# Kernel optimization log

Hardware: AMD Instinct MI355X
Metric: run time of the kernel (lower is better)

## Reference

```python
import jax, jax.numpy as jnp
import numpy as np

S, E, K, D = 50000, 20000, 128, 64
NUM_LAYER = 3
E1, E0 = 1000000, 1000000  # nnz of pos / neg adjacency
B = 4096


def _edges(key, n_rows, n_cols, n_edges):
    k1, k2, k3 = jax.random.split(key, 3)
    rows = jax.random.randint(k1, (n_edges,), 0, n_rows)
    cols = jax.random.randint(k2, (n_edges,), 0, n_cols)
    vals = jax.random.uniform(k3, (n_edges,), jnp.float32, 0.0, 0.1)
    return rows, cols, vals


def setup_inputs() -> dict:
    key = jax.random.key(0)
    ks = jax.random.split(key, 32)
    inp = {}
    inp['stu_id'] = jax.random.randint(ks[0], (B,), 0, S)
    inp['exer_id'] = jax.random.randint(ks[1], (B,), 0, E)
    inp['kn_emb'] = (jax.random.uniform(ks[2], (B, K)) < 0.1).astype(jnp.float32)
    # embeddings
    inp['stu_emb'] = jax.random.normal(ks[3], (S, D), jnp.float32) * 0.1
    inp['exer_emb'] = jax.random.normal(ks[4], (E, D), jnp.float32) * 0.1
    inp['kn_base'] = jax.random.normal(ks[5], (K, D), jnp.float32) * 0.1
    inp['stu_bias'] = jax.random.normal(ks[6], (S, 1), jnp.float32) * 0.1
    inp['e_disc'] = jax.random.normal(ks[7], (E, 1), jnp.float32) * 0.1
    # GCN linear layers
    inp['W1_w'] = jax.random.normal(ks[8], (K, K), jnp.float32) * (1.0 / np.sqrt(K))
    inp['W1_b'] = jnp.zeros((K,), jnp.float32)
    inp['W0_w'] = jax.random.normal(ks[9], (K, K), jnp.float32) * (1.0 / np.sqrt(K))
    inp['W0_b'] = jnp.zeros((K,), jnp.float32)
    # PosLinear prednet
    inp['pn1_w'] = jax.random.normal(ks[10], (256, K), jnp.float32) * 0.05
    inp['pn1_b'] = jnp.zeros((256,), jnp.float32)
    inp['pn2_w'] = jax.random.normal(ks[11], (128, 256), jnp.float32) * 0.05
    inp['pn2_b'] = jnp.zeros((128,), jnp.float32)
    inp['pn3_w'] = jax.random.normal(ks[12], (1, 128), jnp.float32) * 0.05
    inp['pn3_b'] = jnp.zeros((1,), jnp.float32)
    # sparse adjacencies (COO) pos(1) / neg(0), user->item and item->user
    r, c, v = _edges(ks[13], S, E, E1)
    inp['ui1_r'], inp['ui1_c'], inp['ui1_v'] = r, c, v
    r, c, v = _edges(ks[14], E, S, E1)
    inp['iu1_r'], inp['iu1_c'], inp['iu1_v'] = r, c, v
    r, c, v = _edges(ks[15], S, E, E0)
    inp['ui0_r'], inp['ui0_c'], inp['ui0_v'] = r, c, v
    r, c, v = _edges(ks[16], E, S, E0)
    inp['iu0_r'], inp['iu0_c'], inp['iu0_v'] = r, c, v
    # self-loop degree normalizers (1/(deg+1)-style positive scalars)
    inp['d_i_1'] = jax.random.uniform(ks[17], (S,), jnp.float32, 0.01, 1.0)
    inp['d_j_1'] = jax.random.uniform(ks[18], (E,), jnp.float32, 0.01, 1.0)
    inp['d_i_0'] = jax.random.uniform(ks[19], (S,), jnp.float32, 0.01, 1.0)
    inp['d_j_0'] = jax.random.uniform(ks[20], (E,), jnp.float32, 0.01, 1.0)
    return inp


def _spmm(rows, cols, vals, x, n_rows):
    # sparse [n_rows, n_cols] @ dense [n_cols, K]
    return jax.ops.segment_sum(vals[:, None] * x[cols], rows, num_segments=n_rows)


def _poslinear(x, w, b):
    wp = 2.0 * jax.nn.relu(-w) + w  # == |w|, as in PosLinear
    return x @ wp.T + b


def reference(stu_id, exer_id, kn_emb, stu_emb, exer_emb, kn_base, stu_bias, e_disc,
              W1_w, W1_b, W0_w, W0_b, pn1_w, pn1_b, pn2_w, pn2_b, pn3_w, pn3_b,
              ui1_r, ui1_c, ui1_v, iu1_r, iu1_c, iu1_v,
              ui0_r, ui0_c, ui0_v, iu0_r, iu0_c, iu0_v,
              d_i_1, d_j_1, d_i_0, d_j_0):
    # project embeddings onto knowledge space: [S,K], [E,K]
    stat = stu_emb @ kn_base.T
    kdiff = exer_emb @ kn_base.T
    for _ in range(NUM_LAYER):
        u1 = _spmm(ui1_r, ui1_c, ui1_v, kdiff, S) + stat * d_i_1[:, None]
        u1 = u1 @ W1_w.T + W1_b
        i1 = _spmm(iu1_r, iu1_c, iu1_v, stat, E) + kdiff * d_j_1[:, None]
        i1 = i1 @ W1_w.T + W1_b
        u0 = _spmm(ui0_r, ui0_c, ui0_v, kdiff, S) + stat * d_i_0[:, None]
        u0 = u0 @ W0_w.T + W0_b
        i0 = _spmm(iu0_r, iu0_c, iu0_v, stat, E) + kdiff * d_j_0[:, None]
        i0 = i0 @ W0_w.T + W0_b
        stat = u1 + u0
        kdiff = i1 + i0
    # diagnosis head (NCD-style), dropout in eval mode -> identity
    stat_b = jax.nn.sigmoid(stat[stu_id] + stu_bias[stu_id])      # [B,K]
    k_d = jax.nn.sigmoid(kdiff[exer_id])                           # [B,K]
    disc = jax.nn.sigmoid(e_disc[exer_id])                         # [B,1]
    x = disc * (stat_b - k_d) * kn_emb
    x = jax.nn.sigmoid(_poslinear(x, pn1_w, pn1_b))
    x = jax.nn.sigmoid(_poslinear(x, pn2_w, pn2_b))
    out = jax.nn.sigmoid(_poslinear(x, pn3_w, pn3_b)).reshape(-1)
    return out
```

## Files before the change

### kernel.cpp

```cpp
#include <hip/hip_runtime.h>
#include <hip/hip_bf16.h>

#define SN 50000
#define EN 20000
#define KN 128
#define DN 64
#define BN 4096
#define NE 1000000
#define NLAYER 3

#define CH_SHIFT 12
#define NCH0 5
#define NCH1 13
#define SIDE1_BASE2 (2 * SN * NCH0)
#define NTOT2 (2 * (SN * NCH0 + EN * NCH1))

#define BIN_SHIFT 11
#define NBIN2 ((NTOT2 + 2047) >> 11)
#define T1 4096
#define PG1 ((NE + T1 - 1) / T1)
#define HB 256

typedef float f32x4 __attribute__((ext_vector_type(4)));
typedef float f32x2 __attribute__((ext_vector_type(2)));
typedef short bf16x8 __attribute__((ext_vector_type(8)));

__device__ __forceinline__ float sigmoidf_(float v) { return 1.f / (1.f + __expf(-v)); }
__device__ __forceinline__ float bf_lo(unsigned u) { return __uint_as_float(u << 16); }
__device__ __forceinline__ float bf_hi(unsigned u) { return __uint_as_float(u & 0xffff0000u); }
__device__ __forceinline__ float bf_one(unsigned short s) { return __uint_as_float((unsigned)s << 16); }
__device__ __forceinline__ unsigned packbf2(float a, float b) {
    __hip_bfloat16 ha = __float2bfloat16(a), hb = __float2bfloat16(b);
    unsigned short ua = *(unsigned short*)&ha, ub = *(unsigned short*)&hb;
    return (unsigned)ua | ((unsigned)ub << 16);
}
__device__ __forceinline__ unsigned short packbf1(float a) {
    __hip_bfloat16 ha = __float2bfloat16(a);
    return *(unsigned short*)&ha;
}

struct CsrB {
    const int* rows[4]; const int* cols[4]; const float* vals[4];
};

__device__ __forceinline__ int bucket_idx(int a, int r, int cc) {
    int side = a >> 1;
    int nch = side ? NCH1 : NCH0;
    int base = side ? SIDE1_BASE2 : 0;
    int tb = a & 1;
    return base + (2 * r + tb) * nch + (cc >> CH_SHIFT);
}

__global__ __launch_bounds__(256) void hist_coarse(CsrB c, int* __restrict__ cnt) {
    __shared__ int h[512];
    const int t = threadIdx.x;
    h[t] = 0; h[t + 256] = 0;
    __syncthreads();
    const int a = blockIdx.x >> 8;
    const int tile = blockIdx.x & 255;
    const int per = (NE + HB - 1) / HB;
    const int beg = tile * per, end = min(beg + per, NE);
    for (int i = beg + t; i < end; i += 256)
        atomicAdd(&h[bucket_idx(a, c.rows[a][i], c.cols[a][i]) >> BIN_SHIFT], 1);
    __syncthreads();
    if (h[t]) atomicAdd(&cnt[t], h[t]);
    if (h[t + 256]) atomicAdd(&cnt[t + 256], h[t + 256]);
}

__global__ __launch_bounds__(512) void scan_coarse(const int* __restrict__ cnt,
                                                   int* __restrict__ base,
                                                   int* __restrict__ tails) {
    __shared__ int sh[512];
    const int t = threadIdx.x;
    const int v = (t < NBIN2) ? cnt[t] : 0;
    sh[t] = v;
    __syncthreads();
    for (int o = 1; o < 512; o <<= 1) {
        int x = sh[t]; int u = (t >= o) ? sh[t - o] : 0;
        __syncthreads(); sh[t] = x + u; __syncthreads();
    }
    if (t < NBIN2) {
        const int ex = sh[t] - v;
        base[t] = ex;
        tails[t] = ex;
    }
    if (t == 511) base[NBIN2] = sh[511];
}

__global__ __launch_bounds__(512) void part1(CsrB c, int* __restrict__ tails,
                                             int2* __restrict__ stg) {
    __shared__ int2 srec[T1];
    __shared__ unsigned short sbin[T1];
    __shared__ int h[512], offs[512], gbase[512], sc[512];
    const int t = threadIdx.x;
    const int a = blockIdx.x / PG1;
    const int tile = blockIdx.x - a * PG1;
    const int beg = tile * T1;
    const int cnt = min(T1, NE - beg);
    h[t] = 0;
    __syncthreads();

    int2 rec[8]; int rbin[8]; int rrank[8];
#pragma unroll
    for (int k = 0; k < 8; ++k) {
        int o = t + k * 512;
        if (o < cnt) {
            int i = beg + o;
            int cc = c.cols[a][i];
            int B = bucket_idx(a, c.rows[a][i], cc);
            int bin = B >> BIN_SHIFT;
            rec[k] = make_int2(cc | ((B & 2047) << 17), __float_as_int(c.vals[a][i]));
            rbin[k] = bin;
            rrank[k] = atomicAdd(&h[bin], 1);
        } else {
            rbin[k] = -1;
        }
    }
    __syncthreads();
    sc[t] = h[t];
    __syncthreads();
    for (int o = 1; o < 512; o <<= 1) {
        int x = sc[t]; int u = (t >= o) ? sc[t - o] : 0;
        __syncthreads(); sc[t] = x + u; __syncthreads();
    }
    offs[t] = sc[t] - h[t];
    if (h[t] > 0) gbase[t] = atomicAdd(&tails[t], h[t]);
    __syncthreads();
#pragma unroll
    for (int k = 0; k < 8; ++k) {
        if (rbin[k] >= 0) {
            int pos = offs[rbin[k]] + rrank[k];
            srec[pos] = rec[k];
            sbin[pos] = (unsigned short)rbin[k];
        }
    }
    __syncthreads();
    for (int idx = t; idx < cnt; idx += 512) {
        int b = sbin[idx];
        stg[gbase[b] + (idx - offs[b])] = srec[idx];
    }
}

__global__ __launch_bounds__(512) void part2(const int* __restrict__ coarseBase,
                                             const int2* __restrict__ stg,
                                             int* __restrict__ rp,
                                             int2* __restrict__ cv) {
    __shared__ int cnt2[2048];
    __shared__ int tsum[512];
    const int b = blockIdx.x;
    const int t = threadIdx.x;
    const int fineBase = b << BIN_SHIFT;
    const int nf = min(2048, NTOT2 - fineBase);
    const int segBeg = coarseBase[b];
    const int segEnd = coarseBase[b + 1];
    for (int i = t; i < 2048; i += 512) cnt2[i] = 0;
    __syncthreads();
    for (int e = segBeg + t; e < segEnd; e += 512)
        atomicAdd(&cnt2[((unsigned)stg[e].x) >> 17], 1);
    __syncthreads();
    const int i4 = t * 4;
    int v0 = cnt2[i4], v1 = cnt2[i4 + 1], v2 = cnt2[i4 + 2], v3 = cnt2[i4 + 3];
    tsum[t] = v0 + v1 + v2 + v3;
    __syncthreads();
    for (int o = 1; o < 512; o <<= 1) {
        int x = tsum[t]; int u = (t >= o) ? tsum[t - o] : 0;
        __syncthreads(); tsum[t] = x + u; __syncthreads();
    }
    const int pre = (t == 0) ? 0 : tsum[t - 1];
    const int p0 = pre, p1 = pre + v0, p2 = p1 + v1, p3 = p2 + v2;
    cnt2[i4] = p0; cnt2[i4 + 1] = p1; cnt2[i4 + 2] = p2; cnt2[i4 + 3] = p3;
    if (i4 + 0 < nf) rp[fineBase + i4 + 0] = segBeg + p0;
    if (i4 + 1 < nf) rp[fineBase + i4 + 1] = segBeg + p1;
    if (i4 + 2 < nf) rp[fineBase + i4 + 2] = segBeg + p2;
    if (i4 + 3 < nf) rp[fineBase + i4 + 3] = segBeg + p3;
    if (b == NBIN2 - 1 && t == 511) rp[NTOT2] = segEnd;
    __syncthreads();
    for (int e = segBeg + t; e < segEnd; e += 512) {
        int2 r = stg[e];
        int pos = segBeg + atomicAdd(&cnt2[((unsigned)r.x) >> 17], 1);
        cv[pos] = make_int2(r.x & 0xFFFF, r.y);
    }
}

__global__ __launch_bounds__(256) void f2bf(const float* __restrict__ src,
                                            unsigned short* __restrict__ dst, int n2) {
    int i = blockIdx.x * 256 + threadIdx.x;
    if (i < n2) {
        float2 f = ((const float2*)src)[i];
        ((unsigned*)dst)[i] = packbf2(f.x, f.y);
    }
}

__global__ __launch_bounds__(256) void bf2fp8(const unsigned* __restrict__ src,
                                              unsigned* __restrict__ dst, int n4) {
    int i = blockIdx.x * 256 + threadIdx.x;
    if (i < n4) {
        unsigned a = src[2 * i], b = src[2 * i + 1];
        float f0 = bf_lo(a), f1 = bf_hi(a), f2 = bf_lo(b), f3 = bf_hi(b);
        int pk = __builtin_amdgcn_cvt_pk_fp8_f32(f0, f1, 0, false);
        pk = __builtin_amdgcn_cvt_pk_fp8_f32(f2, f3, pk, true);
        dst[i] = (unsigned)pk;
    }
}

template <int KK>
__global__ __launch_bounds__(256) void gemm_proj(const float* __restrict__ X,
                                                 const unsigned short* __restrict__ W,
                                                 unsigned short* __restrict__ out, int M) {
    constexpr int PITCH = KK + 8;
    __shared__ unsigned short Wl[128 * PITCH];
    const int t = threadIdx.x;
    for (int idx = t * 8; idx < 128 * KK; idx += 2048) {
        int r = idx / KK, k = idx - r * KK;
        *(uint4*)(&Wl[r * PITCH + k]) = *(const uint4*)(&W[idx]);
    }
    __syncthreads();
    const int lane = t & 63;
    const int nm = lane & 15;
    const int quad = lane >> 4;
    const int row0 = blockIdx.x * 64 + (t >> 6) * 16;
    if (row0 >= M) return;

    f32x4 acc[8];
#pragma unroll
    for (int nt = 0; nt < 8; ++nt) acc[nt] = (f32x4){0.f, 0.f, 0.f, 0.f};

    const float* xrow = X + (size_t)(row0 + nm) * KK + quad * 8;
#pragma unroll
    for (int ks = 0; ks < KK / 32; ++ks) {
        float4 f0 = *(const float4*)(xrow + ks * 32);
        float4 f1 = *(const float4*)(xrow + ks * 32 + 4);
        unsigned q[4] = {packbf2(f0.x, f0.y), packbf2(f0.z, f0.w),
                         packbf2(f1.x, f1.y), packbf2(f1.z, f1.w)};
        bf16x8 a = *(bf16x8*)q;
#pragma unroll
        for (int nt = 0; nt < 8; ++nt) {
            bf16x8 b = *(const bf16x8*)(&Wl[(nt * 16 + nm) * PITCH + ks * 32 + quad * 8]);
            acc[nt] = __builtin_amdgcn_mfma_f32_16x16x32_bf16(a, b, acc[nt], 0, 0, 0);
        }
    }
    unsigned short* orow = out + (size_t)(row0 + quad * 4) * 128 + nm;
#pragma unroll
    for (int r = 0; r < 4; ++r)
#pragma unroll
        for (int nt = 0; nt < 8; ++nt)
            orow[(size_t)r * 128 + nt * 16] = packbf1(acc[nt][r]);
}

template <bool LIST>
__global__ __launch_bounds__(256) void gemm2_mfma(
    const unsigned short* __restrict__ agg1S, const unsigned short* __restrict__ agg0S,
    const unsigned short* __restrict__ yS,
    const float* __restrict__ d1S, const float* __restrict__ d0S,
    unsigned short* __restrict__ outS,
    const unsigned short* __restrict__ agg1E, const unsigned short* __restrict__ agg0E,
    const unsigned short* __restrict__ yE,
    const float* __restrict__ d1E, const float* __restrict__ d0E,
    unsigned short* __restrict__ outE,
    const unsigned short* __restrict__ W1, const unsigned short* __restrict__ W0,
    const float* __restrict__ b1, const float* __restrict__ b0,
    const int* __restrict__ idsS, const int* __restrict__ idsE, int nblkS) {
    constexpr int PITCH = 136;
    __shared__ unsigned short Wl[2 * 128 * PITCH];
    const int t = threadIdx.x;
    for (int idx = t * 8; idx < 128 * 128; idx += 2048) {
        int r = idx >> 7, k = idx & 127;
        *(uint4*)(&Wl[r * PITCH + k]) = *(const uint4*)(&W1[idx]);
        *(uint4*)(&Wl[128 * PITCH + r * PITCH + k]) = *(const uint4*)(&W0[idx]);
    }
    __syncthreads();
    const bool sideE = (int)blockIdx.x >= nblkS;
    const unsigned short* agg1 = sideE ? agg1E : agg1S;
    const unsigned short* agg0 = sideE ? agg0E : agg0S;
    const unsigned short* y    = sideE ? yE : yS;
    const float* d1 = sideE ? d1E : d1S;
    const float* d0 = sideE ? d0E : d0S;
    unsigned short* out = sideE ? outE : outS;
    const int M = LIST ? BN : (sideE ? EN : SN);
    const int lane = t & 63;
    const int nm = lane & 15;
    const int quad = lane >> 4;
    const int row0 = ((int)blockIdx.x - (sideE ? nblkS : 0)) * 64 + (t >> 6) * 16;
    if (row0 >= M) return;

    const int lrow = row0 + nm;
    int grow = lrow;
    if (LIST) grow = (sideE ? idsE : idsS)[lrow];

    const float d1v = d1[grow];
    const float d0v = d0[grow];

    f32x4 acc[8];
#pragma unroll
    for (int nt = 0; nt < 8; ++nt) acc[nt] = (f32x4){0.f, 0.f, 0.f, 0.f};

    const size_t rbA = (size_t)lrow * 128 + quad * 8;
    const size_t rbY = (size_t)grow * 128 + quad * 8;
#pragma unroll
    for (int ks = 0; ks < 4; ++ks) {
        uint4 ua1 = *(const uint4*)(agg1 + rbA + ks * 32);
        uint4 ua0 = *(const uint4*)(agg0 + rbA + ks * 32);
        uint4 uy  = *(const uint4*)(y    + rbY + ks * 32);
        uint4 p1, p0;
        {
            unsigned* a1 = (unsigned*)&ua1; unsigned* a0 = (unsigned*)&ua0;
            unsigned* yy = (unsigned*)&uy;
            unsigned* q1 = (unsigned*)&p1; unsigned* q0 = (unsigned*)&p0;
#pragma unroll
            for (int w = 0; w < 4; ++w) {
                float ylo = bf_lo(yy[w]), yhi = bf_hi(yy[w]);
                q1[w] = packbf2(bf_lo(a1[w]) + d1v * ylo, bf_hi(a1[w]) + d1v * yhi);
                q0[w] = packbf2(bf_lo(a0[w]) + d0v * ylo, bf_hi(a0[w]) + d0v * yhi);
            }
        }
        bf16x8 af1 = *(bf16x8*)&p1;
        bf16x8 af0 = *(bf16x8*)&p0;
#pragma unroll
        for (int nt = 0; nt < 8; ++nt) {
            bf16x8 bw1 = *(const bf16x8*)(&Wl[(nt * 16 + nm) * PITCH + ks * 32 + quad * 8]);
            acc[nt] = __builtin_amdgcn_mfma_f32_16x16x32_bf16(af1, bw1, acc[nt], 0, 0, 0);
            bf16x8 bw0 = *(const bf16x8*)(&Wl[128 * PITCH + (nt * 16 + nm) * PITCH + ks * 32 + quad * 8]);
            acc[nt] = __builtin_amdgcn_mfma_f32_16x16x32_bf16(af0, bw0, acc[nt], 0, 0, 0);
        }
    }
    unsigned short* orow = out + (size_t)(row0 + quad * 4) * 128 + nm;
#pragma unroll
    for (int nt = 0; nt < 8; ++nt) {
        float bb = b1[nt * 16 + nm] + b0[nt * 16 + nm];
#pragma unroll
        for (int r = 0; r < 4; ++r)
            orow[(size_t)r * 128 + nt * 16] = packbf1(acc[nt][r] + bb);
    }
}

template <bool LIST>
__global__ __launch_bounds__(256) void spmm_all(
    const int* __restrict__ rp, const long long* __restrict__ cv,
    const unsigned char* __restrict__ kd8, const unsigned char* __restrict__ st8,
    unsigned short* __restrict__ as1, unsigned short* __restrict__ as0,
    unsigned short* __restrict__ ae1, unsigned short* __restrict__ ae0,
    const int* __restrict__ idsS, const int* __restrict__ idsE) {
    const int wave = (blockIdx.x * 256 + threadIdx.x) >> 6;
    const int lane = threadIdx.x & 63;
    const int NW = LIST ? 2 * BN : SN + EN;
    if (wave >= NW) return;
    const bool sideE = LIST ? (wave >= BN) : (wave >= SN);
    const int li = sideE ? (wave - (LIST ? BN : SN)) : wave;
    const int r = LIST ? (sideE ? idsE[li] : idsS[li]) : li;
    const int nch = sideE ? NCH1 : NCH0;
    const int* rpb = rp + (sideE ? SIDE1_BASE2 : 0);
    const int q = lane >> 4;
    const int c = lane & 15;
    const unsigned char* g8 = (sideE ? st8 : kd8) + c * 8;

    const int rbase = 2 * r * nch;
    const int e0 = rpb[rbase];
    const int em = rpb[rbase + nch];
    const int ee = rpb[rbase + 2 * nch];

    f32x2 accP[4], accN[4];
#pragma unroll
    for (int j = 0; j < 4; ++j) { accP[j] = (f32x2){0.f, 0.f}; accN[j] = (f32x2){0.f, 0.f}; }

#define QUAD(E, ACC)                                                        \
    {                                                                       \
        int col = (int)((E) & 0xFFFF);                                      \
        float v = __int_as_float((int)((E) >> 32));                         \
        f32x2 vv = {v, v};                                                  \
        uint2 u = *(const uint2*)(g8 + (col << 7));                         \
        ACC[0] += vv * __builtin_amdgcn_cvt_pk_f32_fp8((int)u.x, false);    \
        ACC[1] += vv * __builtin_amdgcn_cvt_pk_f32_fp8((int)u.x, true);     \
        ACC[2] += vv * __builtin_amdgcn_cvt_pk_f32_fp8((int)u.y, false);    \
        ACC[3] += vv * __builtin_amdgcn_cvt_pk_f32_fp8((int)u.y, true);     \
    }

    {
        int e = e0;
        for (; e + 16 <= em; e += 16) {
            long long E0 = cv[e + q];
            long long E1 = cv[e + 4 + q];
            long long E2 = cv[e + 8 + q];
            long long E3 = cv[e + 12 + q];
            QUAD(E0, accP) QUAD(E1, accP) QUAD(E2, accP) QUAD(E3, accP)
        }
        for (; e + 4 <= em; e += 4) {
            long long E0 = cv[e + q];
            QUAD(E0, accP)
        }
        if (e < em) {
            int idx = min(e + q, em - 1);
            long long E0 = cv[idx];
            if (e + q >= em) E0 &= 0xFFFFLL;
            QUAD(E0, accP)
        }
    }
    {
        int e = em;
        for (; e + 16 <= ee; e += 16) {
            long long E0 = cv[e + q];
            long long E1 = cv[e + 4 + q];
            long long E2 = cv[e + 8 + q];
            long long E3 = cv[e + 12 + q];
            QUAD(E0, accN) QUAD(E1, accN) QUAD(E2, accN) QUAD(E3, accN)
        }
        for (; e + 4 <= ee; e += 4) {
            long long E0 = cv[e + q];
            QUAD(E0, accN)
        }
        if (e < ee) {
            int idx = min(e + q, ee - 1);
            long long E0 = cv[idx];
            if (e + q >= ee) E0 &= 0xFFFFLL;
            QUAD(E0, accN)
        }
    }
#undef QUAD

#pragma unroll
    for (int j = 0; j < 4; ++j) {
        accP[j].x += __shfl_xor(accP[j].x, 16);
        accP[j].y += __shfl_xor(accP[j].y, 16);
        accN[j].x += __shfl_xor(accN[j].x, 16);
        accN[j].y += __shfl_xor(accN[j].y, 16);
        accP[j].x += __shfl_xor(accP[j].x, 32);
        accP[j].y += __shfl_xor(accP[j].y, 32);
        accN[j].x += __shfl_xor(accN[j].x, 32);
        accN[j].y += __shfl_xor(accN[j].y, 32);
    }
    unsigned short* o1 = sideE ? ae1 : as1;
    unsigned short* o0 = sideE ? ae0 : as0;
    const int oi = LIST ? li : r;
    const int base = (oi << 7) + c * 8;
    if (q == 0) {
        uint4 w;
        w.x = packbf2(accP[0].x, accP[0].y);
        w.y = packbf2(accP[1].x, accP[1].y);
        w.z = packbf2(accP[2].x, accP[2].y);
        w.w = packbf2(accP[3].x, accP[3].y);
        *(uint4*)&o1[base] = w;
    } else if (q == 1) {
        uint4 w;
        w.x = packbf2(accN[0].x, accN[0].y);
        w.y = packbf2(accN[1].x, accN[1].y);
        w.z = packbf2(accN[2].x, accN[2].y);
        w.w = packbf2(accN[3].x, accN[3].y);
        *(uint4*)&o0[base] = w;
    }
}

template <int KK, int NCOLS, int ROWS, bool ABSW, bool SIG>
__global__ __launch_bounds__(256) void gemm_xwT(const float* __restrict__ X,
                                                const float* __restrict__ W,
                                                const float* __restrict__ bias,
                                                float* __restrict__ out, int M) {
    constexpr int KP = 32;
    constexpr int NG = 256 / NCOLS;
    constexpr int RT = ROWS / NG;
    __shared__ float BT[KP * (NCOLS + 1)];
    __shared__ float Xl[ROWS * (KK + 1)];
    const int t = threadIdx.x;
    const int j = t % NCOLS;
    const int rg = t / NCOLS;
    const int row0 = blockIdx.x * ROWS;

    for (int idx = t; idx < ROWS * KK; idx += 256) {
        int r = idx / KK, k = idx % KK;
        int gr = row0 + r;
        Xl[r * (KK + 1) + k] = (gr < M) ? X[gr * KK + k] : 0.f;
    }
    float acc[RT];
#pragma unroll
    for (int i = 0; i < RT; ++i) acc[i] = 0.f;

    for (int k0 = 0; k0 < KK; k0 += KP) {
        __syncthreads();
        for (int idx = t; idx < NCOLS * KP; idx += 256) {
            int jj = idx / KP, kp = idx % KP;
            float w = W[jj * KK + k0 + kp];
            BT[kp * (NCOLS + 1) + jj] = ABSW ? fabsf(w) : w;
        }
        __syncthreads();
#pragma unroll
        for (int kp = 0; kp < KP; ++kp) {
            float b = BT[kp * (NCOLS + 1) + j];
#pragma unroll
            for (int rr = 0; rr < RT; ++rr)
                acc[rr] += Xl[(rg * RT + rr) * (KK + 1) + k0 + kp] * b;
        }
    }
    float bj = bias ? bias[j] : 0.f;
#pragma unroll
    for (int rr = 0; rr < RT; ++rr) {
        int gr = row0 + rg * RT + rr;
        if (gr < M) {
            float v = acc[rr] + bj;
            out[gr * NCOLS + j] = SIG ? sigmoidf_(v) : v;
        }
    }
}

__global__ __launch_bounds__(128) void head1_kernel(
    const int* __restrict__ stu_id, const int* __restrict__ exer_id,
    const float* __restrict__ kn_emb, const unsigned short* __restrict__ statB,
    const unsigned short* __restrict__ kdB, const float* __restrict__ stu_bias,
    const float* __restrict__ e_disc, float* __restrict__ x) {
    const int b = blockIdx.x;
    const int k = threadIdx.x;
    const int sid = stu_id[b], eid = exer_id[b];
    float disc = sigmoidf_(e_disc[eid]);
    float sb = sigmoidf_(bf_one(statB[(b << 7) + k]) + stu_bias[sid]);
    float kd = sigmoidf_(bf_one(kdB[(b << 7) + k]));
    x[(b << 7) + k] = disc * (sb - kd) * kn_emb[(b << 7) + k];
}

__global__ __launch_bounds__(256) void pn3_kernel(const float* __restrict__ h2,
                                                  const float* __restrict__ w3,
                                                  const float* __restrict__ b3,
                                                  float* __restrict__ out) {
    __shared__ float wl[128];
    const int t = threadIdx.x;
    if (t < 128) wl[t] = fabsf(w3[t]);
    __syncthreads();
    const int b = blockIdx.x * 256 + t;
    float acc = 0.f;
#pragma unroll 4
    for (int k = 0; k < 128; ++k) acc += h2[(b << 7) + k] * wl[k];
    out[b] = sigmoidf_(acc + b3[0]);
}

static inline size_t align256(size_t x) { return (x + 255) & ~size_t(255); }

extern "C" void kernel_launch(void* const* d_in, const int* in_sizes, int n_in,
                              void* d_out, int out_size, void* d_ws, size_t ws_size,
                              hipStream_t stream) {
    const int*   stu_id   = (const int*)d_in[0];
    const int*   exer_id  = (const int*)d_in[1];
    const float* kn_emb   = (const float*)d_in[2];
    const float* stu_emb  = (const float*)d_in[3];
    const float* exer_emb = (const float*)d_in[4];
    const float* kn_base  = (const float*)d_in[5];
    const float* stu_bias = (const float*)d_in[6];
    const float* e_disc   = (const float*)d_in[7];
    const float* W1_w     = (const float*)d_in[8];
    const float* W1_b     = (const float*)d_in[9];
    const float* W0_w     = (const float*)d_in[10];
    const float* W0_b     = (const float*)d_in[11];
    const float* pn1_w    = (const float*)d_in[12];
    const float* pn1_b    = (const float*)d_in[13];
    const float* pn2_w    = (const float*)d_in[14];
    const float* pn2_b    = (const float*)d_in[15];
    const float* pn3_w    = (const float*)d_in[16];
    const float* pn3_b    = (const float*)d_in[17];
    const int*   ui1_r = (const int*)d_in[18]; const int* ui1_c = (const int*)d_in[19];
    const float* ui1_v = (const float*)d_in[20];
    const int*   iu1_r = (const int*)d_in[21]; const int* iu1_c = (const int*)d_in[22];
    const float* iu1_v = (const float*)d_in[23];
    const int*   ui0_r = (const int*)d_in[24]; const int* ui0_c = (const int*)d_in[25];
    const float* ui0_v = (const float*)d_in[26];
    const int*   iu0_r = (const int*)d_in[27]; const int* iu0_c = (const int*)d_in[28];
    const float* iu0_v = (const float*)d_in[29];
    const float* d_i_1 = (const float*)d_in[30];
    const float* d_j_1 = (const float*)d_in[31];
    const float* d_i_0 = (const float*)d_in[32];
    const float* d_j_0 = (const float*)d_in[33];
    float* out = (float*)d_out;

    typedef unsigned short u16;
    typedef unsigned char u8;
    char* p = (char*)d_ws;
    size_t off = 0;
    auto alloc = [&](size_t bytes) { char* q = p + off; off += align256(bytes); return q; };
    u16* stat  = (u16*)alloc(size_t(SN) * KN * 2);
    u16* kdiff = (u16*)alloc(size_t(EN) * KN * 2);
    u8* st8 = (u8*)alloc(size_t(SN) * KN);
    u8* kd8 = (u8*)alloc(size_t(EN) * KN);
    u16* as1 = (u16*)alloc(size_t(SN) * KN * 2);
    u16* as0 = (u16*)alloc(size_t(SN) * KN * 2);
    u16* ae1 = (u16*)alloc(size_t(EN) * KN * 2);
    u16* ae0 = (u16*)alloc(size_t(EN) * KN * 2);
    u16* statB = (u16*)alloc(size_t(BN) * KN * 2);
    u16* kdB   = (u16*)alloc(size_t(BN) * KN * 2);
    u16* Kb  = (u16*)alloc(size_t(KN) * DN * 2);
    u16* Wb1 = (u16*)alloc(size_t(KN) * KN * 2);
    u16* Wb0 = (u16*)alloc(size_t(KN) * KN * 2);
    int*  coarseCnt  = (int*)alloc(512 * 4);
    int*  coarseBase = (int*)alloc((NBIN2 + 1) * 4);
    int*  tails      = (int*)alloc(512 * 4);
    int*  rp_all     = (int*)alloc(size_t(NTOT2 + 1) * 4);
    int2* stg        = (int2*)alloc(size_t(4) * NE * 8);
    int2* cv_all     = (int2*)alloc(size_t(4) * NE * 8);
    float* xh = (float*)alloc(size_t(BN) * KN * 4);
    float* h1 = (float*)alloc(size_t(BN) * 256 * 4);
    float* h2 = (float*)alloc(size_t(BN) * 128 * 4);
    if (off > ws_size) return;

    CsrB c;
    c.rows[0] = ui1_r; c.cols[0] = ui1_c; c.vals[0] = ui1_v;
    c.rows[1] = ui0_r; c.cols[1] = ui0_c; c.vals[1] = ui0_v;
    c.rows[2] = iu1_r; c.cols[2] = iu1_c; c.vals[2] = iu1_v;
    c.rows[3] = iu0_r; c.cols[3] = iu0_c; c.vals[3] = iu0_v;

    hipMemsetAsync(coarseCnt, 0, 512 * 4, stream);
    hist_coarse<<<4 * HB, 256, 0, stream>>>(c, coarseCnt);
    scan_coarse<<<1, 512, 0, stream>>>(coarseCnt, coarseBase, tails);
    part1<<<4 * PG1, 512, 0, stream>>>(c, tails, stg);
    part2<<<NBIN2, 512, 0, stream>>>(coarseBase, stg, rp_all, cv_all);

    f2bf<<<(KN * DN / 2 + 255) / 256, 256, 0, stream>>>(kn_base, Kb, KN * DN / 2);
    f2bf<<<(KN * KN / 2 + 255) / 256, 256, 0, stream>>>(W1_w, Wb1, KN * KN / 2);
    f2bf<<<(KN * KN / 2 + 255) / 256, 256, 0, stream>>>(W0_w, Wb0, KN * KN / 2);

    gemm_proj<DN><<<(SN + 63) / 64, 256, 0, stream>>>(stu_emb, Kb, stat, SN);
    gemm_proj<DN><<<(EN + 63) / 64, 256, 0, stream>>>(exer_emb, Kb, kdiff, EN);

    const int N4 = (SN + EN) * KN / 4;
    const int nblkS = (SN + 63) / 64, nblkE = (EN + 63) / 64;

    for (int l = 0; l < NLAYER; ++l) {
        bf2fp8<<<(N4 + 255) / 256, 256, 0, stream>>>((const unsigned*)stat,
                                                     (unsigned*)st8, N4);
        if (l < NLAYER - 1) {
            spmm_all<false><<<(SN + EN + 3) / 4, 256, 0, stream>>>(
                rp_all, (const long long*)cv_all, kd8, st8, as1, as0, ae1, ae0,
                nullptr, nullptr);
            gemm2_mfma<false><<<nblkS + nblkE, 256, 0, stream>>>(
                as1, as0, stat, d_i_1, d_i_0, stat,
                ae1, ae0, kdiff, d_j_1, d_j_0, kdiff,
                Wb1, Wb0, W1_b, W0_b, nullptr, nullptr, nblkS);
        } else {
            spmm_all<true><<<(2 * BN) / 4, 256, 0, stream>>>(
                rp_all, (const long long*)cv_all, kd8, st8, as1, as0, ae1, ae0,
                stu_id, exer_id);
            gemm2_mfma<true><<<2 * (BN / 64), 256, 0, stream>>>(
                as1, as0, stat, d_i_1, d_i_0, statB,
                ae1, ae0, kdiff, d_j_1, d_j_0, kdB,
                Wb1, Wb0, W1_b, W0_b, stu_id, exer_id, BN / 64);
        }
    }

    head1_kernel<<<BN, 128, 0, stream>>>(stu_id, exer_id, kn_emb, statB, kdB,
                                         stu_bias, e_disc, xh);
    gemm_xwT<128, 256, 16, true, true><<<BN / 16, 256, 0, stream>>>(xh, pn1_w, pn1_b, h1, BN);
    gemm_xwT<256, 128, 32, true, true><<<BN / 32, 256, 0, stream>>>(h1, pn2_w, pn2_b, h2, BN);
    pn3_kernel<<<BN / 256, 256, 0, stream>>>(h2, pn3_w, pn3_b, out);
    (void)out_size; (void)n_in; (void)in_sizes;
}
```

Before: 616.3 us.

## Interleave student/exercise row blocks and software-pipeline pos/neg SpMM edge loads

In the full (non-list) SpMM, the block-to-row mapping now interleaves five student-row blocks with two exercise-row blocks in each group of seven. This mixes short and long rows across the grid to balance load and spread memory traffic. A new joint loop walks the positive and negative edge segments together and prefetches the next 8 packed edges of each before processing the current ones. This aims to hide gather and load latency. The prefetch can read past a segment's end, which is safe only if the edge array is padded or followed by valid memory.

```diff
diff --git a/kernel.cpp b/kernel.cpp
--- a/kernel.cpp
+++ b/kernel.cpp
@@ -340,13 +340,22 @@
     unsigned short* __restrict__ as1, unsigned short* __restrict__ as0,
     unsigned short* __restrict__ ae1, unsigned short* __restrict__ ae0,
     const int* __restrict__ idsS, const int* __restrict__ idsE) {
-    const int wave = (blockIdx.x * 256 + threadIdx.x) >> 6;
     const int lane = threadIdx.x & 63;
-    const int NW = LIST ? 2 * BN : SN + EN;
-    if (wave >= NW) return;
-    const bool sideE = LIST ? (wave >= BN) : (wave >= SN);
-    const int li = sideE ? (wave - (LIST ? BN : SN)) : wave;
-    const int r = LIST ? (sideE ? idsE[li] : idsS[li]) : li;
+    bool sideE;
+    int r, li;
+    if (LIST) {
+        const int wave = (blockIdx.x * 256 + threadIdx.x) >> 6;
+        if (wave >= 2 * BN) return;
+        sideE = wave >= BN;
+        li = sideE ? wave - BN : wave;
+        r = (sideE ? idsE : idsS)[li];
+    } else {
+        const int g = blockIdx.x / 7, sub = blockIdx.x - g * 7;
+        sideE = sub >= 5;
+        const int rowblk = sideE ? (g * 2 + sub - 5) : (g * 5 + sub);
+        r = rowblk * 4 + (int)(threadIdx.x >> 6);
+        li = r;
+    }
     const int nch = sideE ? NCH1 : NCH0;
     const int* rpb = rp + (sideE ? SIDE1_BASE2 : 0);
     const int q = lane >> 4;
@@ -374,8 +383,21 @@
         ACC[3] += vv * __builtin_amdgcn_cvt_pk_f32_fp8((int)u.y, true);     \
     }
 
+    int eP = e0, eN = em;
+    if (em - eP >= 8 && ee - eN >= 8) {
+        long long P0 = cv[eP + q], P1 = cv[eP + 4 + q];
+        long long N0 = cv[eN + q], N1 = cv[eN + 4 + q];
+        while (true) {
+            long long P0n = cv[eP + 8 + q], P1n = cv[eP + 12 + q];
+            long long N0n = cv[eN + 8 + q], N1n = cv[eN + 12 + q];
+            QUAD(P0, accP) QUAD(P1, accP) QUAD(N0, accN) QUAD(N1, accN)
+            eP += 8; eN += 8;
+            if (em - eP < 8 || ee - eN < 8) break;
+            P0 = P0n; P1 = P1n; N0 = N0n; N1 = N1n;
+        }
+    }
     {
-        int e = e0;
+        int e = eP;
         for (; e + 16 <= em; e += 16) {
             long long E0 = cv[e + q];
             long long E1 = cv[e + 4 + q];
@@ -395,7 +417,7 @@
         }
     }
     {
-        int e = em;
+        int e = eN;
         for (; e + 16 <= ee; e += 16) {
             long long E0 = cv[e + q];
             long long E1 = cv[e + 4 + q];
```

Result: no change. 621.6 us (+0.9%).

## Fuse fp8 conversion into GEMM epilogues, merge weight casts, use 512-thread gemm2 blocks

Applied to the files above, without the earlier changes.

Removes the standalone per-layer bf16-to-fp8 conversion kernel. The projection and layer GEMM epilogues now write the fp8 copy alongside the bf16 output. The three small weight-cast launches are merged into one kernel. gemm2 blocks grow to 512 threads covering 128 rows, so the weight tile is staged into LDS half as often. The fp8 epilogue writes are byte-granular and strided, which may coalesce poorly, and larger blocks change occupancy.

```diff
diff --git a/kernel.cpp b/kernel.cpp
--- a/kernel.cpp
+++ b/kernel.cpp
@@ -37,6 +37,11 @@
 __device__ __forceinline__ unsigned short packbf1(float a) {
     __hip_bfloat16 ha = __float2bfloat16(a);
     return *(unsigned short*)&ha;
+}
+__device__ __forceinline__ unsigned char fp8_of_bf16(unsigned short h) {
+    float f = bf_one(h);
+    int pk = __builtin_amdgcn_cvt_pk_fp8_f32(f, f, 0, false);
+    return (unsigned char)(pk & 0xff);
 }
 
 struct CsrB {
@@ -182,31 +187,32 @@
     }
 }
 
-__global__ __launch_bounds__(256) void f2bf(const float* __restrict__ src,
-                                            unsigned short* __restrict__ dst, int n2) {
-    int i = blockIdx.x * 256 + threadIdx.x;
-    if (i < n2) {
-        float2 f = ((const float2*)src)[i];
-        ((unsigned*)dst)[i] = packbf2(f.x, f.y);
-    }
-}
-
-__global__ __launch_bounds__(256) void bf2fp8(const unsigned* __restrict__ src,
-                                              unsigned* __restrict__ dst, int n4) {
-    int i = blockIdx.x * 256 + threadIdx.x;
-    if (i < n4) {
-        unsigned a = src[2 * i], b = src[2 * i + 1];
-        float f0 = bf_lo(a), f1 = bf_hi(a), f2 = bf_lo(b), f3 = bf_hi(b);
-        int pk = __builtin_amdgcn_cvt_pk_fp8_f32(f0, f1, 0, false);
-        pk = __builtin_amdgcn_cvt_pk_fp8_f32(f2, f3, pk, true);
-        dst[i] = (unsigned)pk;
-    }
+__global__ __launch_bounds__(256) void f2bf3(
+    const float* __restrict__ s0, unsigned short* __restrict__ d0, int n0,
+    const float* __restrict__ s1, unsigned short* __restrict__ d1, int n1,
+    const float* __restrict__ s2, unsigned short* __restrict__ d2, int n2) {
+    int j = blockIdx.x * 256 + threadIdx.x;
+    const float* s; unsigned short* d;
+    if (j < n0) { s = s0; d = d0; }
+    else {
+        j -= n0;
+        if (j < n1) { s = s1; d = d1; }
+        else {
+            j -= n1;
+            if (j >= n2) return;
+            s = s2; d = d2;
+        }
+    }
+    float2 f = ((const float2*)s)[j];
+    ((unsigned*)d)[j] = packbf2(f.x, f.y);
 }
 
 template <int KK>
 __global__ __launch_bounds__(256) void gemm_proj(const float* __restrict__ X,
                                                  const unsigned short* __restrict__ W,
-                                                 unsigned short* __restrict__ out, int M) {
+                                                 unsigned short* __restrict__ out,
+                                                 unsigned char* __restrict__ f8,
+                                                 int M) {
     constexpr int PITCH = KK + 8;
     __shared__ unsigned short Wl[128 * PITCH];
     const int t = threadIdx.x;
@@ -239,31 +245,36 @@
             acc[nt] = __builtin_amdgcn_mfma_f32_16x16x32_bf16(a, b, acc[nt], 0, 0, 0);
         }
     }
-    unsigned short* orow = out + (size_t)(row0 + quad * 4) * 128 + nm;
+    const size_t obase = (size_t)(row0 + quad * 4) * 128 + nm;
+    unsigned short* orow = out + obase;
+    unsigned char* frow = f8 + obase;
 #pragma unroll
     for (int r = 0; r < 4; ++r)
 #pragma unroll
-        for (int nt = 0; nt < 8; ++nt)
-            orow[(size_t)r * 128 + nt * 16] = packbf1(acc[nt][r]);
+        for (int nt = 0; nt < 8; ++nt) {
+            unsigned short h = packbf1(acc[nt][r]);
+            orow[(size_t)r * 128 + nt * 16] = h;
+            frow[(size_t)r * 128 + nt * 16] = fp8_of_bf16(h);
+        }
 }
 
 template <bool LIST>
-__global__ __launch_bounds__(256) void gemm2_mfma(
+__global__ __launch_bounds__(512) void gemm2_mfma(
     const unsigned short* __restrict__ agg1S, const unsigned short* __restrict__ agg0S,
     const unsigned short* __restrict__ yS,
     const float* __restrict__ d1S, const float* __restrict__ d0S,
-    unsigned short* __restrict__ outS,
+    unsigned short* __restrict__ outS, unsigned char* __restrict__ f8S,
     const unsigned short* __restrict__ agg1E, const unsigned short* __restrict__ agg0E,
     const unsigned short* __restrict__ yE,
     const float* __restrict__ d1E, const float* __restrict__ d0E,
-    unsigned short* __restrict__ outE,
+    unsigned short* __restrict__ outE, unsigned char* __restrict__ f8E,
     const unsigned short* __restrict__ W1, const unsigned short* __restrict__ W0,
     const float* __restrict__ b1, const float* __restrict__ b0,
     const int* __restrict__ idsS, const int* __restrict__ idsE, int nblkS) {
     constexpr int PITCH = 136;
     __shared__ unsigned short Wl[2 * 128 * PITCH];
     const int t = threadIdx.x;
-    for (int idx = t * 8; idx < 128 * 128; idx += 2048) {
+    for (int idx = t * 8; idx < 128 * 128; idx += 4096) {
         int r = idx >> 7, k = idx & 127;
         *(uint4*)(&Wl[r * PITCH + k]) = *(const uint4*)(&W1[idx]);
         *(uint4*)(&Wl[128 * PITCH + r * PITCH + k]) = *(const uint4*)(&W0[idx]);
@@ -276,11 +287,12 @@
     const float* d1 = sideE ? d1E : d1S;
     const float* d0 = sideE ? d0E : d0S;
     unsigned short* out = sideE ? outE : outS;
+    unsigned char* f8 = sideE ? f8E : f8S;
     const int M = LIST ? BN : (sideE ? EN : SN);
     const int lane = t & 63;
     const int nm = lane & 15;
     const int quad = lane >> 4;
-    const int row0 = ((int)blockIdx.x - (sideE ? nblkS : 0)) * 64 + (t >> 6) * 16;
+    const int row0 = ((int)blockIdx.x - (sideE ? nblkS : 0)) * 128 + (t >> 6) * 16;
     if (row0 >= M) return;
 
     const int lrow = row0 + nm;
@@ -323,13 +335,18 @@
             acc[nt] = __builtin_amdgcn_mfma_f32_16x16x32_bf16(af0, bw0, acc[nt], 0, 0, 0);
         }
     }
-    unsigned short* orow = out + (size_t)(row0 + quad * 4) * 128 + nm;
+    const size_t obase = (size_t)(row0 + quad * 4) * 128 + nm;
+    unsigned short* orow = out + obase;
+    unsigned char* frow = f8 + obase;
 #pragma unroll
     for (int nt = 0; nt < 8; ++nt) {
         float bb = b1[nt * 16 + nm] + b0[nt * 16 + nm];
 #pragma unroll
-        for (int r = 0; r < 4; ++r)
-            orow[(size_t)r * 128 + nt * 16] = packbf1(acc[nt][r] + bb);
+        for (int r = 0; r < 4; ++r) {
+            unsigned short h = packbf1(acc[nt][r] + bb);
+            orow[(size_t)r * 128 + nt * 16] = h;
+            if (!LIST) frow[(size_t)r * 128 + nt * 16] = fp8_of_bf16(h);
+        }
     }
 }
 
@@ -606,35 +623,34 @@
     part1<<<4 * PG1, 512, 0, stream>>>(c, tails, stg);
     part2<<<NBIN2, 512, 0, stream>>>(coarseBase, stg, rp_all, cv_all);
 
-    f2bf<<<(KN * DN / 2 + 255) / 256, 256, 0, stream>>>(kn_base, Kb, KN * DN / 2);
-    f2bf<<<(KN * KN / 2 + 255) / 256, 256, 0, stream>>>(W1_w, Wb1, KN * KN / 2);
-    f2bf<<<(KN * KN / 2 + 255) / 256, 256, 0, stream>>>(W0_w, Wb0, KN * KN / 2);
-
-    gemm_proj<DN><<<(SN + 63) / 64, 256, 0, stream>>>(stu_emb, Kb, stat, SN);
-    gemm_proj<DN><<<(EN + 63) / 64, 256, 0, stream>>>(exer_emb, Kb, kdiff, EN);
-
-    const int N4 = (SN + EN) * KN / 4;
-    const int nblkS = (SN + 63) / 64, nblkE = (EN + 63) / 64;
+    {
+        const int n0 = KN * DN / 2, n1 = KN * KN / 2, n2 = KN * KN / 2;
+        f2bf3<<<(n0 + n1 + n2 + 255) / 256, 256, 0, stream>>>(
+            kn_base, Kb, n0, W1_w, Wb1, n1, W0_w, Wb0, n2);
+    }
+
+    gemm_proj<DN><<<(SN + 63) / 64, 256, 0, stream>>>(stu_emb, Kb, stat, st8, SN);
+    gemm_proj<DN><<<(EN + 63) / 64, 256, 0, stream>>>(exer_emb, Kb, kdiff, kd8, EN);
+
+    const int nblkS = (SN + 127) / 128, nblkE = (EN + 127) / 128;
 
     for (int l = 0; l < NLAYER; ++l) {
-        bf2fp8<<<(N4 + 255) / 256, 256, 0, stream>>>((const unsigned*)stat,
-                                                     (unsigned*)st8, N4);
         if (l < NLAYER - 1) {
             spmm_all<false><<<(SN + EN + 3) / 4, 256, 0, stream>>>(
                 rp_all, (const long long*)cv_all, kd8, st8, as1, as0, ae1, ae0,
                 nullptr, nullptr);
-            gemm2_mfma<false><<<nblkS + nblkE, 256, 0, stream>>>(
-                as1, as0, stat, d_i_1, d_i_0, stat,
-                ae1, ae0, kdiff, d_j_1, d_j_0, kdiff,
+            gemm2_mfma<false><<<nblkS + nblkE, 512, 0, stream>>>(
+                as1, as0, stat, d_i_1, d_i_0, stat, st8,
+                ae1, ae0, kdiff, d_j_1, d_j_0, kdiff, kd8,
                 Wb1, Wb0, W1_b, W0_b, nullptr, nullptr, nblkS);
         } else {
             spmm_all<true><<<(2 * BN) / 4, 256, 0, stream>>>(
                 rp_all, (const long long*)cv_all, kd8, st8, as1, as0, ae1, ae0,
                 stu_id, exer_id);
-            gemm2_mfma<true><<<2 * (BN / 64), 256, 0, stream>>>(
-                as1, as0, stat, d_i_1, d_i_0, statB,
-                ae1, ae0, kdiff, d_j_1, d_j_0, kdB,
-                Wb1, Wb0, W1_b, W0_b, stu_id, exer_id, BN / 64);
+            gemm2_mfma<true><<<2 * (BN / 128), 512, 0, stream>>>(
+                as1, as0, stat, d_i_1, d_i_0, statB, nullptr,
+                ae1, ae0, kdiff, d_j_1, d_j_0, kdB, nullptr,
+                Wb1, Wb0, W1_b, W0_b, stu_id, exer_id, BN / 128);
         }
     }
 
```

After: 607.1 us. About the same (-1.5%).
